# Kernel optimization log

Hardware: AMD Instinct MI355X
Metric: run time of the kernel (lower is better)

Reference implementation:

```python
import jax, jax.numpy as jnp
import numpy as np

EPS = 1e-5
NEG_SLOPE = 0.2
GN_GROUPS = 8


def conv2d(x, w, b):
    # x: [B,C,H,W], w: [O,I,3,3]
    y = jax.lax.conv_general_dilated(
        x, w, window_strides=(1, 1), padding=((1, 1), (1, 1)),
        dimension_numbers=('NCHW', 'OIHW', 'NCHW'))
    return y + b[None, :, None, None]


def conv3d_d(x, w, b):
    # x: [B,C,D,H,W], w: [O,I,3,1,1] -> conv along D only
    y = jax.lax.conv_general_dilated(
        x, w, window_strides=(1, 1, 1), padding=((1, 1), (0, 0), (0, 0)),
        dimension_numbers=('NCDHW', 'OIDHW', 'NCDHW'))
    return y + b[None, :, None, None, None]


def group_norm(x, gamma, beta):
    # x: [B,C,D,H,W]; normalize per group over (C/g, D, H, W)
    B, C, D, H, W = x.shape
    xg = x.reshape(B, GN_GROUPS, C // GN_GROUPS, D, H, W)
    mu = jnp.mean(xg, axis=(2, 3, 4, 5), keepdims=True)
    var = jnp.var(xg, axis=(2, 3, 4, 5), keepdims=True)
    xn = ((xg - mu) * jax.lax.rsqrt(var + EPS)).reshape(B, C, D, H, W)
    return xn * gamma[None, :, None, None, None] + beta[None, :, None, None, None]


def setup_inputs() -> dict:
    key = jax.random.key(0)
    ks = jax.random.split(key, 8)
    C = 32
    B, D, H, W = 2, 24, 160, 160
    s = lambda fan: 1.0 / np.sqrt(fan)
    return {
        'x': jax.random.normal(ks[0], (B, C, D, H, W), jnp.float32),
        'w_f1': jax.random.normal(ks[1], (2 * C, C, 3, 1, 1), jnp.float32) * s(C * 3),
        'b_f1': jnp.zeros((2 * C,), jnp.float32),
        'gn_g': jnp.ones((2 * C,), jnp.float32),
        'gn_b': jnp.zeros((2 * C,), jnp.float32),
        'w_f2': jax.random.normal(ks[2], (C, 2 * C, 3, 1, 1), jnp.float32) * s(2 * C * 3),
        'b_f2': jnp.zeros((C,), jnp.float32),
        'w_u': jax.random.normal(ks[3], (C, 2 * C, 3, 3), jnp.float32) * s(2 * C * 9),
        'b_u': jnp.zeros((C,), jnp.float32),
        'w_r': jax.random.normal(ks[4], (C, 2 * C, 3, 3), jnp.float32) * s(2 * C * 9),
        'b_r': jnp.zeros((C,), jnp.float32),
        'w_o': jax.random.normal(ks[5], (C, 2 * C, 3, 3), jnp.float32) * s(2 * C * 9),
        'b_o': jnp.zeros((C,), jnp.float32),
    }


def reference(x, w_f1, b_f1, gn_g, gn_b, w_f2, b_f2, w_u, b_u, w_r, b_r, w_o, b_o):
    B, C, D, H, W = x.shape

    # slice_flow: Conv3d(C->2C,(3,1,1)) -> GroupNorm(8) -> LeakyReLU(0.2) -> Conv3d(2C->C,(3,1,1))
    sf = conv3d_d(x, w_f1, b_f1)
    sf = group_norm(sf, gn_g, gn_b)
    sf = jnp.where(sf >= 0, sf, NEG_SLOPE * sf)
    slice_features = conv3d_d(sf, w_f2, b_f2)

    def gru_step(h, xd):
        combined = jnp.concatenate([xd, h], axis=1)
        update = jax.nn.sigmoid(conv2d(combined, w_u, b_u))
        reset = jax.nn.sigmoid(conv2d(combined, w_r, b_r))
        combined_reset = jnp.concatenate([xd, reset * h], axis=1)
        cand = jnp.tanh(conv2d(combined_reset, w_o, b_o))
        h_new = (1.0 - update) * h + update * cand
        return h_new, h_new

    xd = jnp.moveaxis(x, 2, 0)  # [D,B,C,H,W]
    h0 = jnp.zeros((B, C, H, W), x.dtype)
    _, fwd = jax.lax.scan(gru_step, h0, xd)                 # [D,B,C,H,W]
    _, bwd = jax.lax.scan(gru_step, h0, xd, reverse=True)   # aligned with xd order

    enhanced = xd + fwd + bwd                                # [D,B,C,H,W]
    return jnp.moveaxis(enhanced, 0, 2) + slice_features
```

## Files before the change

### kernel.cpp

```cpp
#include <hip/hip_runtime.h>
#include <hip/hip_bf16.h>
#include <stdint.h>

#define EPS_GN 1e-5f
#define NEG_SLOPE 0.2f

static constexpr int  Bn   = 2;
static constexpr int  Cn   = 32;
static constexpr int  Dn   = 24;
static constexpr int  Hn   = 160;
static constexpr int  Wn   = 160;
static constexpr int  HWn  = Hn * Wn;
static constexpr long DHWn = (long)Dn * HWn;
static constexpr long NPIX = (long)Bn * Dn * HWn;

using frag8  = __attribute__((ext_vector_type(8)))  short;
using accf16 = __attribute__((ext_vector_type(16))) float;

__device__ __forceinline__ float bf2f(__hip_bfloat16 v) { return __bfloat162float(v); }
__device__ __forceinline__ __hip_bfloat16 f2bf(float v) { return __float2bfloat16(v); }
__device__ __forceinline__ float sigm(float v) { return 1.f / (1.f + __expf(-v)); }
__device__ __forceinline__ float tanh_(float v) {
    float e = __expf(2.f * v);
    return 1.f - 2.f / (e + 1.f);
}

__global__ __launch_bounds__(256) void wtrans_kernel(
    const float* __restrict__ src, float* __restrict__ dst, int O, int IK)
{
    int i = blockIdx.x * 256 + threadIdx.x;
    if (i >= O * IK) return;
    int o = i / IK, ik = i - o * IK;
    dst[ik * O + o] = src[i];
}

__global__ __launch_bounds__(256) void bpack_kernel(
    const float* __restrict__ w, __hip_bfloat16* __restrict__ dst)
{
    int t = blockIdx.x * 256 + threadIdx.x;
    if (t >= 9 * 4 * 64 * 8) return;
    int j    = t & 7;
    int lane = (t >> 3) & 63;
    int kb   = (t >> 9) & 3;
    int tap  = t >> 11;
    int ci   = kb * 16 + (lane >> 5) * 8 + j;
    int o    = lane & 31;
    dst[t] = f2bf(w[(o * 64 + ci) * 9 + tap]);
}

__global__ __launch_bounds__(256) void tohwc_kernel(
    const float* __restrict__ x, __hip_bfloat16* __restrict__ xhwc)
{
    __shared__ float tile[32][65];
    int bd = blockIdx.y;
    int b  = bd / Dn, d = bd % Dn;
    int p0 = blockIdx.x * 64;
    const float* xb = x + (long)b * Cn * DHWn + (long)d * HWn + p0;
    for (int e = threadIdx.x; e < 2048; e += 256) {
        int c = e >> 6, p = e & 63;
        tile[c][p] = xb[(long)c * DHWn + p];
    }
    __syncthreads();
    __hip_bfloat16* ob = xhwc + ((long)bd * HWn + p0) * 32;
    for (int e = threadIdx.x; e < 2048; e += 256) {
        int p = e >> 5, c = e & 31;
        ob[p * 32 + c] = f2bf(tile[c][p]);
    }
}

__global__ __launch_bounds__(256) void conv1_kernel(
    const float* __restrict__ x,
    const float* __restrict__ w1T,
    const float* __restrict__ b1,
    __hip_bfloat16* __restrict__ A)
{
    long idx = (long)blockIdx.x * 256 + threadIdx.x;
    if (idx >= NPIX) return;
    int p  = (int)(idx % HWn);
    int bd = (int)(idx / HWn);
    int d  = bd % Dn;
    int b  = bd / Dn;

    float acc[64];
#pragma unroll
    for (int o = 0; o < 64; o++) acc[o] = b1[o];

    for (int kd = 0; kd < 3; kd++) {
        int dd = d + kd - 1;
        if (dd < 0 || dd >= Dn) continue;
        const float* xp = x + (long)b * Cn * DHWn + (long)dd * HWn + p;
        for (int ci = 0; ci < 32; ci++) {
            float v = xp[(long)ci * DHWn];
            const float* wp = w1T + (ci * 3 + kd) * 64;
#pragma unroll
            for (int o = 0; o < 64; o++) acc[o] += wp[o] * v;
        }
    }
    __hip_bfloat16* Ap = A + (long)b * 64 * DHWn + (long)d * HWn + p;
#pragma unroll
    for (int o = 0; o < 64; o++) Ap[(long)o * DHWn] = f2bf(acc[o]);
}

__global__ __launch_bounds__(256) void stats_kernel(
    const __hip_bfloat16* __restrict__ A, float* __restrict__ gsum, float* __restrict__ gsq)
{
    int slab = blockIdx.y;
    const __hip_bfloat16* base = A + (long)slab * 8 * DHWn + (long)blockIdx.x * 32768;
    float s = 0.f, q = 0.f;
    for (int i = threadIdx.x; i < 32768; i += 256) {
        float v = bf2f(base[i]);
        s += v;
        q += v * v;
    }
    __shared__ float rs_[256], rq_[256];
    int tid = threadIdx.x;
    rs_[tid] = s; rq_[tid] = q;
    __syncthreads();
    for (int st = 128; st > 0; st >>= 1) {
        if (tid < st) { rs_[tid] += rs_[tid + st]; rq_[tid] += rq_[tid + st]; }
        __syncthreads();
    }
    if (tid == 0) {
        atomicAdd(&gsum[slab], rs_[0]);
        atomicAdd(&gsq[slab],  rq_[0]);
    }
}

__global__ __launch_bounds__(128) void finalize_kernel(
    const float* __restrict__ gsum, const float* __restrict__ gsq,
    const float* __restrict__ gn_g, const float* __restrict__ gn_b,
    float* __restrict__ scale, float* __restrict__ shift)
{
    int t = threadIdx.x;
    if (t >= 128) return;
    int b = t >> 6, ci = t & 63, g = ci >> 3;
    float N   = 8.0f * (float)DHWn;
    float mu  = gsum[b * 8 + g] / N;
    float var = gsq[b * 8 + g] / N - mu * mu;
    float rs  = rsqrtf(var + EPS_GN);
    float sc  = rs * gn_g[ci];
    scale[t] = sc;
    shift[t] = gn_b[ci] - mu * sc;
}

__global__ __launch_bounds__(256) void conv2_kernel(
    const __hip_bfloat16* __restrict__ A,
    const float* __restrict__ w2T,
    const float* __restrict__ b2,
    const float* __restrict__ scale, const float* __restrict__ shift,
    const float* __restrict__ x,
    float* __restrict__ out)
{
    long idx = (long)blockIdx.x * 256 + threadIdx.x;
    if (idx >= NPIX) return;
    int p  = (int)(idx % HWn);
    int bd = (int)(idx / HWn);
    int d  = bd % Dn;
    int b  = bd / Dn;

    float acc[32];
#pragma unroll
    for (int o = 0; o < 32; o++) acc[o] = b2[o];

    const float* scb = scale + b * 64;
    const float* shb = shift + b * 64;

    for (int kd = 0; kd < 3; kd++) {
        int dd = d + kd - 1;
        if (dd < 0 || dd >= Dn) continue;
        const __hip_bfloat16* Ap = A + (long)b * 64 * DHWn + (long)dd * HWn + p;
        for (int ci = 0; ci < 64; ci++) {
            float a  = bf2f(Ap[(long)ci * DHWn]);
            float an = a * scb[ci] + shb[ci];
            an = an >= 0.f ? an : NEG_SLOPE * an;
            const float* wp = w2T + (ci * 3 + kd) * 32;
#pragma unroll
            for (int o = 0; o < 32; o++) acc[o] += wp[o] * an;
        }
    }
    const float* xp = x   + (long)b * Cn * DHWn + (long)d * HWn + p;
    float*       op = out + (long)b * Cn * DHWn + (long)d * HWn + p;
#pragma unroll
    for (int o = 0; o < 32; o++)
        op[(long)o * DHWn] = acc[o] + xp[(long)o * DHWn];
}

__global__ __launch_bounds__(256) void gru_gates_mfma(
    const __hip_bfloat16* __restrict__ xhwc,
    int dfwd, int dbwd,
    const __hip_bfloat16* __restrict__ hbf,
    const __hip_bfloat16* __restrict__ Bu,
    const __hip_bfloat16* __restrict__ Br,
    const float* __restrict__ bu, const float* __restrict__ br,
    float* __restrict__ ufrag,
    __hip_bfloat16* __restrict__ rhbf)
{
    int db   = blockIdx.y;
    int dir  = db >> 1, b = db & 1;
    int d    = dir ? dbwd : dfwd;
    int wave = threadIdx.x >> 6;
    int lane = threadIdx.x & 63;
    int ml   = lane & 31;
    int kh   = lane >> 5;

    const __hip_bfloat16* xb = xhwc + ((long)b * Dn + d) * HWn * 32;
    const __hip_bfloat16* hb = hbf  + (long)db * HWn * 32;

    int tile0 = blockIdx.x * 8 + wave * 2;
    int tb[2]   = { tile0 * 32, tile0 * 32 + 32 };
    int py0[2]  = { tb[0] / Wn, tb[1] / Wn };
    int px0[2]  = { tb[0] % Wn, tb[1] % Wn };

    accf16 au[2], ar[2];
#pragma unroll
    for (int t = 0; t < 2; t++)
#pragma unroll
        for (int i = 0; i < 16; i++) { au[t][i] = 0.f; ar[t][i] = 0.f; }

    for (int tap = 0; tap < 9; tap++) {
        int dy = tap / 3 - 1, dx = tap % 3 - 1;
        long poff[2]; bool ok[2];
#pragma unroll
        for (int t = 0; t < 2; t++) {
            int yy = py0[t] + dy;
            int xx = px0[t] + ml + dx;
            ok[t]   = ((unsigned)yy < (unsigned)Hn) & ((unsigned)xx < (unsigned)Wn);
            poff[t] = ((long)(yy * Wn + xx)) * 32;
        }
#pragma unroll
        for (int kb = 0; kb < 4; kb++) {
            frag8 bu_f = *(const frag8*)(Bu + ((tap * 4 + kb) * 64 + lane) * 8);
            frag8 br_f = *(const frag8*)(Br + ((tap * 4 + kb) * 64 + lane) * 8);
            int ch = kb * 16 + kh * 8;
            const __hip_bfloat16* bsel = (kb < 2) ? (xb + ch) : (hb + (ch - 32));
#pragma unroll
            for (int t = 0; t < 2; t++) {
                frag8 a = {};
                if (ok[t]) a = *(const frag8*)(bsel + poff[t]);
                au[t] = __builtin_amdgcn_mfma_f32_32x32x16_bf16(a, bu_f, au[t], 0, 0, 0);
                ar[t] = __builtin_amdgcn_mfma_f32_32x32x16_bf16(a, br_f, ar[t], 0, 0, 0);
            }
        }
    }

    int ch = ml;
    float bias_u = bu[ch], bias_r = br[ch];
#pragma unroll
    for (int t = 0; t < 2; t++) {
        int pb = tb[t];
        float* uf = ufrag + ((long)db * 800 + tile0 + t) * 1024 + lane * 16;
        __hip_bfloat16* rhb = rhbf + (long)db * HWn * 32;
#pragma unroll
        for (int i = 0; i < 16; i++) {
            int row = (i & 3) + 8 * (i >> 2) + 4 * kh;
            int pix = pb + row;
            float hp = bf2f(hb[(long)pix * 32 + ch]);
            float uu = sigm(au[t][i] + bias_u);
            float rr = sigm(ar[t][i] + bias_r);
            uf[i] = uu;
            rhb[(long)pix * 32 + ch] = f2bf(rr * hp);
        }
    }
}

__global__ __launch_bounds__(256) void gru_cand_mfma(
    const __hip_bfloat16* __restrict__ xhwc,
    int dfwd, int dbwd,
    const __hip_bfloat16* __restrict__ rhbf,
    const __hip_bfloat16* __restrict__ Bo,
    const float* __restrict__ bo,
    const float* __restrict__ ufrag,
    __hip_bfloat16* __restrict__ hbf,
    float* __restrict__ out)
{
    int db   = blockIdx.y;
    int dir  = db >> 1, b = db & 1;
    int d    = dir ? dbwd : dfwd;
    int wave = threadIdx.x >> 6;
    int lane = threadIdx.x & 63;
    int ml   = lane & 31;
    int kh   = lane >> 5;

    const __hip_bfloat16* xb  = xhwc + ((long)b * Dn + d) * HWn * 32;
    const __hip_bfloat16* rhb = rhbf + (long)db * HWn * 32;
    __hip_bfloat16*       hb  = hbf  + (long)db * HWn * 32;

    int tile0 = blockIdx.x * 8 + wave * 2;
    int tb[2]   = { tile0 * 32, tile0 * 32 + 32 };
    int py0[2]  = { tb[0] / Wn, tb[1] / Wn };
    int px0[2]  = { tb[0] % Wn, tb[1] % Wn };

    accf16 ao[2];
#pragma unroll
    for (int t = 0; t < 2; t++)
#pragma unroll
        for (int i = 0; i < 16; i++) ao[t][i] = 0.f;

    for (int tap = 0; tap < 9; tap++) {
        int dy = tap / 3 - 1, dx = tap % 3 - 1;
        long poff[2]; bool ok[2];
#pragma unroll
        for (int t = 0; t < 2; t++) {
            int yy = py0[t] + dy;
            int xx = px0[t] + ml + dx;
            ok[t]   = ((unsigned)yy < (unsigned)Hn) & ((unsigned)xx < (unsigned)Wn);
            poff[t] = ((long)(yy * Wn + xx)) * 32;
        }
#pragma unroll
        for (int kb = 0; kb < 4; kb++) {
            frag8 bo_f = *(const frag8*)(Bo + ((tap * 4 + kb) * 64 + lane) * 8);
            int ch = kb * 16 + kh * 8;
            const __hip_bfloat16* bsel = (kb < 2) ? (xb + ch) : (rhb + (ch - 32));
#pragma unroll
            for (int t = 0; t < 2; t++) {
                frag8 a = {};
                if (ok[t]) a = *(const frag8*)(bsel + poff[t]);
                ao[t] = __builtin_amdgcn_mfma_f32_32x32x16_bf16(a, bo_f, ao[t], 0, 0, 0);
            }
        }
    }

    int ch = ml;
    float bias_o = bo[ch];
#pragma unroll
    for (int t = 0; t < 2; t++) {
        int pb = tb[t];
        const float* uf = ufrag + ((long)db * 800 + tile0 + t) * 1024 + lane * 16;
        float* ob = out + ((long)b * Cn + ch) * DHWn + (long)d * HWn;
#pragma unroll
        for (int i = 0; i < 16; i++) {
            int row = (i & 3) + 8 * (i >> 2) + 4 * kh;
            int pix = pb + row;
            float c  = tanh_(ao[t][i] + bias_o);
            float uu = uf[i];
            float hp = bf2f(hb[(long)pix * 32 + ch]);
            float hn = (1.f - uu) * hp + uu * c;
            hb[(long)pix * 32 + ch] = f2bf(hn);
            ob[pix] += hn;
        }
    }
}

extern "C" void kernel_launch(void* const* d_in, const int* in_sizes, int n_in,
                              void* d_out, int out_size, void* d_ws, size_t ws_size,
                              hipStream_t stream)
{
    const float* x    = (const float*)d_in[0];
    const float* w_f1 = (const float*)d_in[1];
    const float* b_f1 = (const float*)d_in[2];
    const float* gn_g = (const float*)d_in[3];
    const float* gn_b = (const float*)d_in[4];
    const float* w_f2 = (const float*)d_in[5];
    const float* b_f2 = (const float*)d_in[6];
    const float* w_u  = (const float*)d_in[7];
    const float* b_u  = (const float*)d_in[8];
    const float* w_r  = (const float*)d_in[9];
    const float* b_r  = (const float*)d_in[10];
    const float* w_o  = (const float*)d_in[11];
    const float* b_o  = (const float*)d_in[12];
    float* out = (float*)d_out;

    char* ws = (char*)d_ws;
    float* w1T  = (float*)ws;
    float* w2T  = w1T + 64 * 96;
    float* gsum = w2T + 32 * 192;
    float* gsq  = gsum + 16;
    float* scal = gsq + 16;
    float* shft = scal + 128;
    __hip_bfloat16* Bu = (__hip_bfloat16*)(shft + 128);
    __hip_bfloat16* Br = Bu + 18432;
    __hip_bfloat16* Bo = Br + 18432;
    char* big = (char*)(Bo + 18432);
    big = (char*)(((uintptr_t)big + 255) & ~(uintptr_t)255);

    __hip_bfloat16* A = (__hip_bfloat16*)big;
    __hip_bfloat16* xhwc  = (__hip_bfloat16*)big;
    __hip_bfloat16* hbf   = (__hip_bfloat16*)(big + 78643200L);
    __hip_bfloat16* rhbf  = (__hip_bfloat16*)(big + 85196800L);
    float*          ufrag = (float*)        (big + 91750400L);

    size_t need = (size_t)(big - ws) + 157286400UL;
    if (ws_size < need) return;

    auto tr = [&](const float* s, float* dst, int O, int IK) {
        int n = O * IK;
        wtrans_kernel<<<(n + 255) / 256, 256, 0, stream>>>(s, dst, O, IK);
    };
    tr(w_f1, w1T, 64, 96);
    tr(w_f2, w2T, 32, 192);
    bpack_kernel<<<72, 256, 0, stream>>>(w_u, Bu);
    bpack_kernel<<<72, 256, 0, stream>>>(w_r, Br);
    bpack_kernel<<<72, 256, 0, stream>>>(w_o, Bo);

    conv1_kernel<<<(int)(NPIX / 256), 256, 0, stream>>>(x, w1T, b_f1, A);
    hipMemsetAsync(gsum, 0, 32 * sizeof(float), stream);
    stats_kernel<<<dim3(150, 16), 256, 0, stream>>>(A, gsum, gsq);
    finalize_kernel<<<1, 128, 0, stream>>>(gsum, gsq, gn_g, gn_b, scal, shft);
    conv2_kernel<<<(int)(NPIX / 256), 256, 0, stream>>>(A, w2T, b_f2, scal, shft, x, out);

    tohwc_kernel<<<dim3(400, Bn * Dn), 256, 0, stream>>>(x, xhwc);
    hipMemsetAsync(hbf, 0, 6553600, stream);

    for (int s = 0; s < Dn; s++) {
        int dfwd = s, dbwd = Dn - 1 - s;
        gru_gates_mfma<<<dim3(100, 4), 256, 0, stream>>>(
            xhwc, dfwd, dbwd, hbf, Bu, Br, b_u, b_r, ufrag, rhbf);
        gru_cand_mfma<<<dim3(100, 4), 256, 0, stream>>>(
            xhwc, dfwd, dbwd, rhbf, Bo, b_o, ufrag, hbf, out);
    }
}
```

Before: 2.327 ms.

## Move slice-flow depth convolutions to bf16 MFMA on channels-last input with fused stats

New measurement: 2.153 ms. 7.5% less time.

```diff
diff --git a/kernel.cpp b/kernel.cpp
--- a/kernel.cpp
+++ b/kernel.cpp
@@ -25,13 +25,36 @@
     return 1.f - 2.f / (e + 1.f);
 }
 
-__global__ __launch_bounds__(256) void wtrans_kernel(
-    const float* __restrict__ src, float* __restrict__ dst, int O, int IK)
-{
-    int i = blockIdx.x * 256 + threadIdx.x;
-    if (i >= O * IK) return;
-    int o = i / IK, ik = i - o * IK;
-    dst[ik * O + o] = src[i];
+__global__ __launch_bounds__(256) void bpack1_kernel(
+    const float* __restrict__ w, __hip_bfloat16* __restrict__ dst)
+{
+    int t = blockIdx.x * 256 + threadIdx.x;
+    if (t >= 6 * 2 * 64 * 8) return;
+    int j    = t & 7;
+    int lane = (t >> 3) & 63;
+    int idx  = t >> 9;
+    int nt   = idx & 1;
+    int kb   = idx >> 1;
+    int o    = nt * 32 + (lane & 31);
+    int k    = kb * 16 + (lane >> 5) * 8 + j;
+    int ci   = k & 31;
+    int kd   = k >> 5;
+    dst[t] = f2bf(w[(o * 32 + ci) * 3 + kd]);
+}
+
+__global__ __launch_bounds__(256) void bpack2_kernel(
+    const float* __restrict__ w, __hip_bfloat16* __restrict__ dst)
+{
+    int t = blockIdx.x * 256 + threadIdx.x;
+    if (t >= 12 * 64 * 8) return;
+    int j    = t & 7;
+    int lane = (t >> 3) & 63;
+    int kb   = t >> 9;
+    int o    = lane & 31;
+    int k    = kb * 16 + (lane >> 5) * 8 + j;
+    int ci   = k & 63;
+    int kd   = k >> 6;
+    dst[t] = f2bf(w[(o * 64 + ci) * 3 + kd]);
 }
 
 __global__ __launch_bounds__(256) void bpack_kernel(
@@ -68,121 +91,203 @@
     }
 }
 
-__global__ __launch_bounds__(256) void conv1_kernel(
-    const float* __restrict__ x,
-    const float* __restrict__ w1T,
+__global__ __launch_bounds__(256) void conv1_mfma(
+    const __hip_bfloat16* __restrict__ xhwc,
+    const __hip_bfloat16* __restrict__ Bp1,
     const float* __restrict__ b1,
-    __hip_bfloat16* __restrict__ A)
-{
-    long idx = (long)blockIdx.x * 256 + threadIdx.x;
-    if (idx >= NPIX) return;
-    int p  = (int)(idx % HWn);
-    int bd = (int)(idx / HWn);
-    int d  = bd % Dn;
-    int b  = bd / Dn;
-
-    float acc[64];
-#pragma unroll
-    for (int o = 0; o < 64; o++) acc[o] = b1[o];
+    int b,
+    __hip_bfloat16* __restrict__ A,
+    float* __restrict__ gsum, float* __restrict__ gsq)
+{
+    int wave = threadIdx.x >> 6;
+    int lane = threadIdx.x & 63;
+    int ml   = lane & 31;
+    int kh   = lane >> 5;
+    int tile0 = blockIdx.x * 8 + wave * 2;
+
+    frag8 bf[6][2];
+#pragma unroll
+    for (int kb = 0; kb < 6; kb++)
+#pragma unroll
+        for (int nt = 0; nt < 2; nt++)
+            bf[kb][nt] = *(const frag8*)(Bp1 + ((kb * 2 + nt) * 64 + lane) * 8);
+
+    int d  = tile0 / 800;
+    int p0 = (tile0 % 800) * 32;
+
+    accf16 acc[2][2];
+#pragma unroll
+    for (int t = 0; t < 2; t++)
+#pragma unroll
+        for (int nt = 0; nt < 2; nt++)
+#pragma unroll
+            for (int i = 0; i < 16; i++) acc[t][nt][i] = 0.f;
 
     for (int kd = 0; kd < 3; kd++) {
         int dd = d + kd - 1;
-        if (dd < 0 || dd >= Dn) continue;
-        const float* xp = x + (long)b * Cn * DHWn + (long)dd * HWn + p;
-        for (int ci = 0; ci < 32; ci++) {
-            float v = xp[(long)ci * DHWn];
-            const float* wp = w1T + (ci * 3 + kd) * 64;
-#pragma unroll
-            for (int o = 0; o < 64; o++) acc[o] += wp[o] * v;
-        }
-    }
-    __hip_bfloat16* Ap = A + (long)b * 64 * DHWn + (long)d * HWn + p;
-#pragma unroll
-    for (int o = 0; o < 64; o++) Ap[(long)o * DHWn] = f2bf(acc[o]);
-}
-
-__global__ __launch_bounds__(256) void stats_kernel(
-    const __hip_bfloat16* __restrict__ A, float* __restrict__ gsum, float* __restrict__ gsq)
-{
-    int slab = blockIdx.y;
-    const __hip_bfloat16* base = A + (long)slab * 8 * DHWn + (long)blockIdx.x * 32768;
-    float s = 0.f, q = 0.f;
-    for (int i = threadIdx.x; i < 32768; i += 256) {
-        float v = bf2f(base[i]);
-        s += v;
-        q += v * v;
-    }
-    __shared__ float rs_[256], rq_[256];
-    int tid = threadIdx.x;
-    rs_[tid] = s; rq_[tid] = q;
+        bool valid = (unsigned)dd < (unsigned)Dn;
+        const __hip_bfloat16* rp = xhwc + ((long)(b * Dn + dd) * HWn) * 32;
+#pragma unroll
+        for (int h2 = 0; h2 < 2; h2++) {
+            int kb = kd * 2 + h2;
+#pragma unroll
+            for (int t = 0; t < 2; t++) {
+                frag8 a = {};
+                if (valid)
+                    a = *(const frag8*)(rp + (long)(p0 + t * 32 + ml) * 32 + h2 * 16 + kh * 8);
+                acc[t][0] = __builtin_amdgcn_mfma_f32_32x32x16_bf16(a, bf[kb][0], acc[t][0], 0, 0, 0);
+                acc[t][1] = __builtin_amdgcn_mfma_f32_32x32x16_bf16(a, bf[kb][1], acc[t][1], 0, 0, 0);
+            }
+        }
+    }
+
+    float bias[2] = { b1[ml], b1[32 + ml] };
+    float s[2] = {0.f, 0.f}, q[2] = {0.f, 0.f};
+    __hip_bfloat16* Ap = A + (long)d * HWn * 64;
+#pragma unroll
+    for (int t = 0; t < 2; t++) {
+        int pb = p0 + t * 32;
+#pragma unroll
+        for (int nt = 0; nt < 2; nt++) {
+#pragma unroll
+            for (int i = 0; i < 16; i++) {
+                int row = (i & 3) + 8 * (i >> 2) + 4 * kh;
+                float v = acc[t][nt][i] + bias[nt];
+                Ap[(long)(pb + row) * 64 + nt * 32 + ml] = f2bf(v);
+                s[nt] += v;
+                q[nt] += v * v;
+            }
+        }
+    }
+#pragma unroll
+    for (int nt = 0; nt < 2; nt++) {
+        s[nt] += __shfl_xor(s[nt], 32);
+        q[nt] += __shfl_xor(q[nt], 32);
+    }
+    __shared__ float ss[64], sq[64];
+    if (threadIdx.x < 64) { ss[threadIdx.x] = 0.f; sq[threadIdx.x] = 0.f; }
     __syncthreads();
-    for (int st = 128; st > 0; st >>= 1) {
-        if (tid < st) { rs_[tid] += rs_[tid + st]; rq_[tid] += rq_[tid + st]; }
-        __syncthreads();
-    }
-    if (tid == 0) {
-        atomicAdd(&gsum[slab], rs_[0]);
-        atomicAdd(&gsq[slab],  rq_[0]);
-    }
-}
-
-__global__ __launch_bounds__(128) void finalize_kernel(
+    if (lane < 32) {
+        atomicAdd(&ss[ml],      s[0]); atomicAdd(&sq[ml],      q[0]);
+        atomicAdd(&ss[32 + ml], s[1]); atomicAdd(&sq[32 + ml], q[1]);
+    }
+    __syncthreads();
+    if (threadIdx.x < 64) {
+        atomicAdd(&gsum[b * 64 + threadIdx.x], ss[threadIdx.x]);
+        atomicAdd(&gsq [b * 64 + threadIdx.x], sq[threadIdx.x]);
+    }
+}
+
+__global__ __launch_bounds__(64) void finalize_kernel(
     const float* __restrict__ gsum, const float* __restrict__ gsq,
     const float* __restrict__ gn_g, const float* __restrict__ gn_b,
-    float* __restrict__ scale, float* __restrict__ shift)
-{
-    int t = threadIdx.x;
-    if (t >= 128) return;
-    int b = t >> 6, ci = t & 63, g = ci >> 3;
+    float* __restrict__ scal, float* __restrict__ shft, int b)
+{
+    int ci = threadIdx.x;
+    if (ci >= 64) return;
+    int g = ci >> 3;
+    float s = 0.f, qq = 0.f;
+#pragma unroll
+    for (int k = 0; k < 8; k++) {
+        s  += gsum[b * 64 + g * 8 + k];
+        qq += gsq [b * 64 + g * 8 + k];
+    }
     float N   = 8.0f * (float)DHWn;
-    float mu  = gsum[b * 8 + g] / N;
-    float var = gsq[b * 8 + g] / N - mu * mu;
+    float mu  = s / N;
+    float var = qq / N - mu * mu;
     float rs  = rsqrtf(var + EPS_GN);
-    float sc  = rs * gn_g[ci];
-    scale[t] = sc;
-    shift[t] = gn_b[ci] - mu * sc;
-}
-
-__global__ __launch_bounds__(256) void conv2_kernel(
-    const __hip_bfloat16* __restrict__ A,
-    const float* __restrict__ w2T,
+    float scv = rs * gn_g[ci];
+    scal[b * 64 + ci] = scv;
+    shft[b * 64 + ci] = gn_b[ci] - mu * scv;
+}
+
+__global__ __launch_bounds__(256) void act_kernel(
+    __hip_bfloat16* __restrict__ A,
+    const float* __restrict__ scal, const float* __restrict__ shft, int b)
+{
+    __shared__ float sc[64], sh[64];
+    if (threadIdx.x < 64) {
+        sc[threadIdx.x] = scal[b * 64 + threadIdx.x];
+        sh[threadIdx.x] = shft[b * 64 + threadIdx.x];
+    }
+    __syncthreads();
+    long i0 = ((long)blockIdx.x * 256 + threadIdx.x) * 8;
+    __hip_bfloat16 loc[8];
+    *(frag8*)loc = *(const frag8*)(A + i0);
+    int c0 = (int)(i0 & 63);
+#pragma unroll
+    for (int j = 0; j < 8; j++) {
+        float f  = bf2f(loc[j]);
+        float an = fmaf(f, sc[c0 + j], sh[c0 + j]);
+        loc[j]   = f2bf(fmaxf(an, NEG_SLOPE * an));
+    }
+    *(frag8*)(A + i0) = *(frag8*)loc;
+}
+
+__global__ __launch_bounds__(256) void conv2_mfma(
+    const __hip_bfloat16* __restrict__ Aact,
+    const __hip_bfloat16* __restrict__ Bp2,
     const float* __restrict__ b2,
-    const float* __restrict__ scale, const float* __restrict__ shift,
     const float* __restrict__ x,
-    float* __restrict__ out)
-{
-    long idx = (long)blockIdx.x * 256 + threadIdx.x;
-    if (idx >= NPIX) return;
-    int p  = (int)(idx % HWn);
-    int bd = (int)(idx / HWn);
-    int d  = bd % Dn;
-    int b  = bd / Dn;
-
-    float acc[32];
-#pragma unroll
-    for (int o = 0; o < 32; o++) acc[o] = b2[o];
-
-    const float* scb = scale + b * 64;
-    const float* shb = shift + b * 64;
+    float* __restrict__ out,
+    int b)
+{
+    int wave = threadIdx.x >> 6;
+    int lane = threadIdx.x & 63;
+    int ml   = lane & 31;
+    int kh   = lane >> 5;
+    int tile0 = blockIdx.x * 8 + wave * 2;
+
+    frag8 bf[12];
+#pragma unroll
+    for (int kb = 0; kb < 12; kb++)
+        bf[kb] = *(const frag8*)(Bp2 + (kb * 64 + lane) * 8);
+
+    int d  = tile0 / 800;
+    int p0 = (tile0 % 800) * 32;
+
+    accf16 acc[2];
+#pragma unroll
+    for (int t = 0; t < 2; t++)
+#pragma unroll
+        for (int i = 0; i < 16; i++) acc[t][i] = 0.f;
 
     for (int kd = 0; kd < 3; kd++) {
         int dd = d + kd - 1;
-        if (dd < 0 || dd >= Dn) continue;
-        const __hip_bfloat16* Ap = A + (long)b * 64 * DHWn + (long)dd * HWn + p;
-        for (int ci = 0; ci < 64; ci++) {
-            float a  = bf2f(Ap[(long)ci * DHWn]);
-            float an = a * scb[ci] + shb[ci];
-            an = an >= 0.f ? an : NEG_SLOPE * an;
-            const float* wp = w2T + (ci * 3 + kd) * 32;
-#pragma unroll
-            for (int o = 0; o < 32; o++) acc[o] += wp[o] * an;
-        }
-    }
-    const float* xp = x   + (long)b * Cn * DHWn + (long)d * HWn + p;
-    float*       op = out + (long)b * Cn * DHWn + (long)d * HWn + p;
-#pragma unroll
-    for (int o = 0; o < 32; o++)
-        op[(long)o * DHWn] = acc[o] + xp[(long)o * DHWn];
+        bool valid = (unsigned)dd < (unsigned)Dn;
+        const __hip_bfloat16* rp = Aact + (long)dd * HWn * 64;
+#pragma unroll
+        for (int qq = 0; qq < 4; qq++) {
+            int kb = kd * 4 + qq;
+#pragma unroll
+            for (int t = 0; t < 2; t++) {
+                frag8 a = {};
+                if (valid)
+                    a = *(const frag8*)(rp + (long)(p0 + t * 32 + ml) * 64 + qq * 16 + kh * 8);
+                acc[t] = __builtin_amdgcn_mfma_f32_32x32x16_bf16(a, bf[kb], acc[t], 0, 0, 0);
+            }
+        }
+    }
+
+    __shared__ float tb[4][32][33];
+    float bias = b2[ml];
+    const float* xb = x   + (long)b * Cn * DHWn + (long)d * HWn;
+    float*       ob = out + (long)b * Cn * DHWn + (long)d * HWn;
+#pragma unroll
+    for (int t = 0; t < 2; t++) {
+        int pb = p0 + t * 32;
+#pragma unroll
+        for (int i = 0; i < 16; i++) {
+            int row = (i & 3) + 8 * (i >> 2) + 4 * kh;
+            tb[wave][row][ml] = acc[t][i] + bias;
+        }
+#pragma unroll
+        for (int r2 = 0; r2 < 16; r2++) {
+            int c = r2 * 2 + kh;
+            float v = tb[wave][ml][c] + xb[(long)c * DHWn + pb + ml];
+            ob[(long)c * DHWn + pb + ml] = v;
+        }
+    }
 }
 
 __global__ __launch_bounds__(256) void gru_gates_mfma(
@@ -361,46 +466,44 @@
     float* out = (float*)d_out;
 
     char* ws = (char*)d_ws;
-    float* w1T  = (float*)ws;
-    float* w2T  = w1T + 64 * 96;
-    float* gsum = w2T + 32 * 192;
-    float* gsq  = gsum + 16;
-    float* scal = gsq + 16;
+    __hip_bfloat16* Bp1 = (__hip_bfloat16*)ws;
+    __hip_bfloat16* Bp2 = Bp1 + 6144;
+    __hip_bfloat16* Bu  = Bp2 + 6144;
+    __hip_bfloat16* Br  = Bu + 18432;
+    __hip_bfloat16* Bo  = Br + 18432;
+    float* gsum = (float*)(Bo + 18432);
+    float* gsq  = gsum + 128;
+    float* scal = gsq + 128;
     float* shft = scal + 128;
-    __hip_bfloat16* Bu = (__hip_bfloat16*)(shft + 128);
-    __hip_bfloat16* Br = Bu + 18432;
-    __hip_bfloat16* Bo = Br + 18432;
-    char* big = (char*)(Bo + 18432);
+    char* big = (char*)(shft + 128);
     big = (char*)(((uintptr_t)big + 255) & ~(uintptr_t)255);
 
-    __hip_bfloat16* A = (__hip_bfloat16*)big;
-    __hip_bfloat16* xhwc  = (__hip_bfloat16*)big;
-    __hip_bfloat16* hbf   = (__hip_bfloat16*)(big + 78643200L);
-    __hip_bfloat16* rhbf  = (__hip_bfloat16*)(big + 85196800L);
-    float*          ufrag = (float*)        (big + 91750400L);
+    __hip_bfloat16* xhwc = (__hip_bfloat16*)big;
+    __hip_bfloat16* Apre = (__hip_bfloat16*)(big + 78643200L);
+    __hip_bfloat16* hbf  = (__hip_bfloat16*)(big + 78643200L);
+    __hip_bfloat16* rhbf = (__hip_bfloat16*)(big + 85196800L);
+    float*          ufrag= (float*)        (big + 91750400L);
 
     size_t need = (size_t)(big - ws) + 157286400UL;
     if (ws_size < need) return;
 
-    auto tr = [&](const float* s, float* dst, int O, int IK) {
-        int n = O * IK;
-        wtrans_kernel<<<(n + 255) / 256, 256, 0, stream>>>(s, dst, O, IK);
-    };
-    tr(w_f1, w1T, 64, 96);
-    tr(w_f2, w2T, 32, 192);
+    bpack1_kernel<<<24, 256, 0, stream>>>(w_f1, Bp1);
+    bpack2_kernel<<<24, 256, 0, stream>>>(w_f2, Bp2);
     bpack_kernel<<<72, 256, 0, stream>>>(w_u, Bu);
     bpack_kernel<<<72, 256, 0, stream>>>(w_r, Br);
     bpack_kernel<<<72, 256, 0, stream>>>(w_o, Bo);
-
-    conv1_kernel<<<(int)(NPIX / 256), 256, 0, stream>>>(x, w1T, b_f1, A);
-    hipMemsetAsync(gsum, 0, 32 * sizeof(float), stream);
-    stats_kernel<<<dim3(150, 16), 256, 0, stream>>>(A, gsum, gsq);
-    finalize_kernel<<<1, 128, 0, stream>>>(gsum, gsq, gn_g, gn_b, scal, shft);
-    conv2_kernel<<<(int)(NPIX / 256), 256, 0, stream>>>(A, w2T, b_f2, scal, shft, x, out);
+    hipMemsetAsync(gsum, 0, 256 * sizeof(float), stream);
 
     tohwc_kernel<<<dim3(400, Bn * Dn), 256, 0, stream>>>(x, xhwc);
+
+    for (int b = 0; b < Bn; b++) {
+        conv1_mfma<<<2400, 256, 0, stream>>>(xhwc, Bp1, b_f1, b, Apre, gsum, gsq);
+        finalize_kernel<<<1, 64, 0, stream>>>(gsum, gsq, gn_g, gn_b, scal, shft, b);
+        act_kernel<<<19200, 256, 0, stream>>>(Apre, scal, shft, b);
+        conv2_mfma<<<2400, 256, 0, stream>>>(Apre, Bp2, b_f2, x, out, b);
+    }
+
     hipMemsetAsync(hbf, 0, 6553600, stream);
-
     for (int s = 0; s < Dn; s++) {
         int dfwd = s, dbwd = Dn - 1 - s;
         gru_gates_mfma<<<dim3(100, 4), 256, 0, stream>>>(
```
